# Optimization experiments

Measured on AMD Instinct MI355X. Metric: run time of the kernel, lower is better.

Reference implementation:

```python
import jax, jax.numpy as jnp
import numpy as np


def pw_dist_sq(X, Y):
    xx = jnp.sum(X * X, axis=1)[:, None]   # [N,1]
    yy = jnp.sum(Y * Y, axis=1)[None, :]   # [1,N]
    xy = X @ Y.T                            # [N,N]
    return jnp.maximum(xx + yy - 2.0 * xy, 0.0)


def setup_inputs() -> dict:
    key = jax.random.key(0)
    k1, k2 = jax.random.split(key)
    N, D = 1024, 128
    X = jax.random.normal(k1, (N, D), dtype=jnp.float32)
    Y = jax.random.normal(k2, (N, D), dtype=jnp.float32)
    return {"X": X, "Y": Y, "h": 1}


def reference(X, Y, h):
    h = float(h)
    inv_h2 = 1.0 / (h * h)
    sq_dists = pw_dist_sq(X, Y)                       # [N,N]
    K = jnp.exp(-0.5 * inv_h2 * sq_dists)             # [N,N]
    # d_K[i,j,:] = -(X[i]-Y[j])/h^2 * K[i,j]; returned reduced over j
    diff = X[:, None, :] - Y[None, :, :]              # [N,N,D]
    d_K_sum = jnp.sum(-diff * inv_h2 * K[:, :, None], axis=1)  # [N,D]
    return K, d_K_sum
```

## Files before the change

kernel.cpp:

```cpp
#include <hip/hip_runtime.h>

#define NN 1024
#define DD 128

typedef float f32x4 __attribute__((ext_vector_type(4)));
typedef _Float16 f16x8 __attribute__((ext_vector_type(8)));

__device__ __forceinline__ f16x8 cvt8(f32x4 a, f32x4 b) {
  f16x8 r;
  r[0] = (_Float16)a.x; r[1] = (_Float16)a.y; r[2] = (_Float16)a.z; r[3] = (_Float16)a.w;
  r[4] = (_Float16)b.x; r[5] = (_Float16)b.y; r[6] = (_Float16)b.z; r[7] = (_Float16)b.w;
  return r;
}

__global__ __launch_bounds__(256) void gk_fused(const float* __restrict__ X,
                                                const float* __restrict__ Y,
                                                const int* __restrict__ hp,
                                                float* __restrict__ out) {
  __shared__ __align__(16) float    Kt[16][132];
  __shared__ __align__(16) _Float16 Ks[16][136];
  __shared__ float yys[128];
  __shared__ unsigned msc[16];
  __shared__ float Sred[16];

  const int tid  = threadIdx.x;
  const int js   = blockIdx.x;
  const int ib   = blockIdx.y;
  const int lane = tid & 63;
  const int w    = tid >> 6;
  const int g    = lane >> 4;
  const int li   = lane & 15;

  const float fh = (float)hp[0];
  const float inv_h2 = 1.0f / (fh * fh);

  if (tid < 16) { msc[tid] = 0u; Sred[tid] = 0.0f; }

  const float* Xr = X + (size_t)(ib * 16 + li) * DD;
  f32x4 xa[4][2];
  float xx = 0.f;
  #pragma unroll
  for (int kt = 0; kt < 4; ++kt) {
    int d0 = kt * 32 + g * 8;
    xa[kt][0] = *(const f32x4*)(Xr + d0);
    xa[kt][1] = *(const f32x4*)(Xr + d0 + 4);
    #pragma unroll
    for (int c = 0; c < 4; ++c)
      xx += xa[kt][0][c] * xa[kt][0][c] + xa[kt][1][c] * xa[kt][1][c];
  }
  xx += __shfl_xor(xx, 16); xx += __shfl_xor(xx, 32);

  const float* Yr0 = Y + (size_t)(js * 128 + w * 32 + li) * DD;
  const float* Yr1 = Yr0 + 16 * DD;
  f32x4 acc0 = {0.f, 0.f, 0.f, 0.f}, acc1 = {0.f, 0.f, 0.f, 0.f};
  float yy0 = 0.f, yy1 = 0.f;
  #pragma unroll
  for (int kt = 0; kt < 4; ++kt) {
    int d0 = kt * 32 + g * 8;
    f32x4 a0 = *(const f32x4*)(Yr0 + d0), b0 = *(const f32x4*)(Yr0 + d0 + 4);
    f32x4 a1 = *(const f32x4*)(Yr1 + d0), b1 = *(const f32x4*)(Yr1 + d0 + 4);
    #pragma unroll
    for (int c = 0; c < 4; ++c) {
      yy0 += a0[c] * a0[c] + b0[c] * b0[c];
      yy1 += a1[c] * a1[c] + b1[c] * b1[c];
    }
    f16x8 bf = cvt8(xa[kt][0], xa[kt][1]);
    acc0 = __builtin_amdgcn_mfma_f32_16x16x32_f16(cvt8(a0, b0), bf, acc0, 0, 0, 0);
    acc1 = __builtin_amdgcn_mfma_f32_16x16x32_f16(cvt8(a1, b1), bf, acc1, 0, 0, 0);
  }
  yy0 += __shfl_xor(yy0, 16); yy0 += __shfl_xor(yy0, 32);
  yy1 += __shfl_xor(yy1, 16); yy1 += __shfl_xor(yy1, 32);
  if (lane < 16) { yys[w * 32 + lane] = yy0; yys[w * 32 + 16 + lane] = yy1; }
  __syncthreads();

  float K[8];
  float m = 0.f, sp = 0.f;
  #pragma unroll
  for (int t = 0; t < 2; ++t) {
    f32x4 a = t ? acc1 : acc0;
    #pragma unroll
    for (int r = 0; r < 4; ++r) {
      int jl = w * 32 + t * 16 + 4 * g + r;
      float e = fminf((a[r] - 0.5f * (xx + yys[jl])) * inv_h2, 0.0f);
      float kv = exp2f(e * 1.44269504088896341f);
      K[t * 4 + r] = kv; m = fmaxf(m, kv); sp += kv;
      Kt[li][jl] = kv;
    }
  }
  m = fmaxf(m, __shfl_xor(m, 16)); m = fmaxf(m, __shfl_xor(m, 32));
  sp += __shfl_xor(sp, 16);        sp += __shfl_xor(sp, 32);
  if (lane < 16) {
    atomicMax(&msc[li], __float_as_uint(m));
    atomicAdd(&Sred[li], sp);
  }
  __syncthreads();

  {
    int i = tid >> 4, seg = tid & 15;
    f32x4 v0 = *(const f32x4*)&Kt[i][seg * 8];
    f32x4 v1 = *(const f32x4*)&Kt[i][seg * 8 + 4];
    float* kb = out + (size_t)(ib * 16 + i) * NN + js * 128 + seg * 8;
    *(f32x4*)kb = v0; *(f32x4*)(kb + 4) = v1;
  }
  {
    unsigned ue = (msc[li] >> 23) & 0xffu;
    unsigned se = 266u - ue; if (se > 254u) se = 254u;
    float scale = __uint_as_float(se << 23);
    #pragma unroll
    for (int t = 0; t < 2; ++t)
      #pragma unroll
      for (int r = 0; r < 4; ++r)
        Ks[li][w * 32 + t * 16 + 4 * g + r] = (_Float16)(K[t * 4 + r] * scale);
  }
  __syncthreads();

  f32x4 c0 = {0.f, 0.f, 0.f, 0.f}, c1 = {0.f, 0.f, 0.f, 0.f};
  const int dA = w * 32 + li;
  const int dB = dA + 16;
  #pragma unroll
  for (int kt = 0; kt < 4; ++kt) {
    f16x8 af = *(const f16x8*)&Ks[li][kt * 32 + g * 8];
    const float* Yb = Y + (size_t)(js * 128 + kt * 32 + g * 8) * DD;
    f16x8 b0, b1;
    #pragma unroll
    for (int e = 0; e < 8; ++e) {
      b0[e] = (_Float16)Yb[e * DD + dA];
      b1[e] = (_Float16)Yb[e * DD + dB];
    }
    c0 = __builtin_amdgcn_mfma_f32_16x16x32_f16(af, b0, c0, 0, 0, 0);
    c1 = __builtin_amdgcn_mfma_f32_16x16x32_f16(af, b1, c1, 0, 0, 0);
  }

  float* dkp = out + (size_t)NN * NN;
  #pragma unroll
  for (int r = 0; r < 4; ++r) {
    int il = 4 * g + r;
    unsigned ue2 = (msc[il] >> 23) & 0xffu;
    unsigned se2 = 266u - ue2; if (se2 > 254u) se2 = 254u;
    float invs = __uint_as_float((254u - se2) << 23);
    float sred = Sred[il];
    int gi = ib * 16 + il;
    float x0 = X[(size_t)gi * DD + dA];
    float x1 = X[(size_t)gi * DD + dB];
    atomicAdd(dkp + (size_t)gi * DD + dA, (c0[r] * invs - sred * x0) * inv_h2);
    atomicAdd(dkp + (size_t)gi * DD + dB, (c1[r] * invs - sred * x1) * inv_h2);
  }
}

extern "C" void kernel_launch(void* const* d_in, const int* in_sizes, int n_in,
                              void* d_out, int out_size, void* d_ws, size_t ws_size,
                              hipStream_t stream) {
  const float* X  = (const float*)d_in[0];
  const float* Y  = (const float*)d_in[1];
  const int*   hp = (const int*)d_in[2];
  float* out = (float*)d_out;

  hipMemsetAsync((void*)(out + (size_t)NN * NN), 0, (size_t)NN * DD * sizeof(float), stream);
  hipLaunchKernelGGL(gk_fused, dim3(8, 64), dim3(256), 0, stream, X, Y, hp, out);
}
```

Before: 20.71 us.

## Replace memset and atomic dK accumulation with workspace partials and reduce kernel

The memset and the global atomicAdd accumulation of d_K_sum are removed. Each block now writes per-column-tile partial products and row sums to a workspace, and a second kernel reduces the 8 partials and applies the X correction. The change also prefetches the Y operand for the second GEMM early, stores K straight from registers instead of staging it through shared memory, and vectorizes the fp16 shared-memory stores. It trades atomic contention and the memset for an extra launch plus about 4MB of workspace traffic.

Measured after the change: 17.36 us. 16.2% less time.

```diff
diff --git a/kernel.cpp b/kernel.cpp
--- a/kernel.cpp
+++ b/kernel.cpp
@@ -4,6 +4,7 @@
 #define DD 128
 
 typedef float f32x4 __attribute__((ext_vector_type(4)));
+typedef _Float16 f16x4 __attribute__((ext_vector_type(4)));
 typedef _Float16 f16x8 __attribute__((ext_vector_type(8)));
 
 __device__ __forceinline__ f16x8 cvt8(f32x4 a, f32x4 b) {
@@ -13,11 +14,13 @@
   return r;
 }
 
-__global__ __launch_bounds__(256) void gk_fused(const float* __restrict__ X,
-                                                const float* __restrict__ Y,
-                                                const int* __restrict__ hp,
-                                                float* __restrict__ out) {
-  __shared__ __align__(16) float    Kt[16][132];
+#define WS_PART 8192
+
+__global__ __launch_bounds__(256, 2) void gk_main(const float* __restrict__ X,
+                                                  const float* __restrict__ Y,
+                                                  const int* __restrict__ hp,
+                                                  float* __restrict__ out,
+                                                  float* __restrict__ ws) {
   __shared__ __align__(16) _Float16 Ks[16][136];
   __shared__ float yys[128];
   __shared__ unsigned msc[16];
@@ -38,16 +41,31 @@
 
   const float* Xr = X + (size_t)(ib * 16 + li) * DD;
   f32x4 xa[4][2];
-  float xx = 0.f;
   #pragma unroll
   for (int kt = 0; kt < 4; ++kt) {
     int d0 = kt * 32 + g * 8;
     xa[kt][0] = *(const f32x4*)(Xr + d0);
     xa[kt][1] = *(const f32x4*)(Xr + d0 + 4);
+  }
+  const int dA = w * 32 + li;
+  const int dB = dA + 16;
+  float bpre0[4][8], bpre1[4][8];
+  #pragma unroll
+  for (int kt = 0; kt < 4; ++kt) {
+    const float* Yb = Y + (size_t)(js * 128 + kt * 32 + g * 8) * DD;
+    #pragma unroll
+    for (int e = 0; e < 8; ++e) {
+      bpre0[kt][e] = Yb[e * DD + dA];
+      bpre1[kt][e] = Yb[e * DD + dB];
+    }
+  }
+
+  float xx = 0.f;
+  #pragma unroll
+  for (int kt = 0; kt < 4; ++kt)
     #pragma unroll
     for (int c = 0; c < 4; ++c)
       xx += xa[kt][0][c] * xa[kt][0][c] + xa[kt][1][c] * xa[kt][1][c];
-  }
   xx += __shfl_xor(xx, 16); xx += __shfl_xor(xx, 32);
 
   const float* Yr0 = Y + (size_t)(js * 128 + w * 32 + li) * DD;
@@ -84,8 +102,14 @@
       float e = fminf((a[r] - 0.5f * (xx + yys[jl])) * inv_h2, 0.0f);
       float kv = exp2f(e * 1.44269504088896341f);
       K[t * 4 + r] = kv; m = fmaxf(m, kv); sp += kv;
-      Kt[li][jl] = kv;
-    }
+    }
+  }
+  {
+    float* kb = out + (size_t)(ib * 16 + li) * NN + js * 128 + w * 32 + 4 * g;
+    f32x4 k0 = { K[0], K[1], K[2], K[3] };
+    f32x4 k1 = { K[4], K[5], K[6], K[7] };
+    *(f32x4*)kb = k0;
+    *(f32x4*)(kb + 16) = k1;
   }
   m = fmaxf(m, __shfl_xor(m, 16)); m = fmaxf(m, __shfl_xor(m, 32));
   sp += __shfl_xor(sp, 16);        sp += __shfl_xor(sp, 32);
@@ -96,55 +120,71 @@
   __syncthreads();
 
   {
-    int i = tid >> 4, seg = tid & 15;
-    f32x4 v0 = *(const f32x4*)&Kt[i][seg * 8];
-    f32x4 v1 = *(const f32x4*)&Kt[i][seg * 8 + 4];
-    float* kb = out + (size_t)(ib * 16 + i) * NN + js * 128 + seg * 8;
-    *(f32x4*)kb = v0; *(f32x4*)(kb + 4) = v1;
-  }
-  {
     unsigned ue = (msc[li] >> 23) & 0xffu;
     unsigned se = 266u - ue; if (se > 254u) se = 254u;
     float scale = __uint_as_float(se << 23);
     #pragma unroll
-    for (int t = 0; t < 2; ++t)
+    for (int t = 0; t < 2; ++t) {
+      f16x4 q;
       #pragma unroll
-      for (int r = 0; r < 4; ++r)
-        Ks[li][w * 32 + t * 16 + 4 * g + r] = (_Float16)(K[t * 4 + r] * scale);
+      for (int r = 0; r < 4; ++r) q[r] = (_Float16)(K[t * 4 + r] * scale);
+      *(f16x4*)&Ks[li][w * 32 + t * 16 + 4 * g] = q;
+    }
   }
   __syncthreads();
 
   f32x4 c0 = {0.f, 0.f, 0.f, 0.f}, c1 = {0.f, 0.f, 0.f, 0.f};
-  const int dA = w * 32 + li;
-  const int dB = dA + 16;
   #pragma unroll
   for (int kt = 0; kt < 4; ++kt) {
     f16x8 af = *(const f16x8*)&Ks[li][kt * 32 + g * 8];
-    const float* Yb = Y + (size_t)(js * 128 + kt * 32 + g * 8) * DD;
     f16x8 b0, b1;
     #pragma unroll
     for (int e = 0; e < 8; ++e) {
-      b0[e] = (_Float16)Yb[e * DD + dA];
-      b1[e] = (_Float16)Yb[e * DD + dB];
+      b0[e] = (_Float16)bpre0[kt][e];
+      b1[e] = (_Float16)bpre1[kt][e];
     }
     c0 = __builtin_amdgcn_mfma_f32_16x16x32_f16(af, b0, c0, 0, 0, 0);
     c1 = __builtin_amdgcn_mfma_f32_16x16x32_f16(af, b1, c1, 0, 0, 0);
   }
 
-  float* dkp = out + (size_t)NN * NN;
+  float* pb = ws + WS_PART + (size_t)js * (NN * DD) + (size_t)(ib * 16) * DD;
   #pragma unroll
   for (int r = 0; r < 4; ++r) {
     int il = 4 * g + r;
     unsigned ue2 = (msc[il] >> 23) & 0xffu;
     unsigned se2 = 266u - ue2; if (se2 > 254u) se2 = 254u;
     float invs = __uint_as_float((254u - se2) << 23);
-    float sred = Sred[il];
-    int gi = ib * 16 + il;
-    float x0 = X[(size_t)gi * DD + dA];
-    float x1 = X[(size_t)gi * DD + dB];
-    atomicAdd(dkp + (size_t)gi * DD + dA, (c0[r] * invs - sred * x0) * inv_h2);
-    atomicAdd(dkp + (size_t)gi * DD + dB, (c1[r] * invs - sred * x1) * inv_h2);
-  }
+    pb[il * DD + dA] = c0[r] * invs;
+    pb[il * DD + dB] = c1[r] * invs;
+  }
+  if (tid < 16) ws[js * NN + ib * 16 + tid] = Sred[tid];
+}
+
+__global__ __launch_bounds__(256) void dk_reduce(const float* __restrict__ X,
+                                                 const int* __restrict__ hp,
+                                                 const float* __restrict__ ws,
+                                                 float* __restrict__ out) {
+  const int unit = blockIdx.x * 256 + threadIdx.x;
+  const int i  = unit >> 5;
+  const int d0 = (unit & 31) * 4;
+  const float fh = (float)hp[0];
+  const float inv_h2 = 1.0f / (fh * fh);
+
+  f32x4 acc = {0.f, 0.f, 0.f, 0.f};
+  float s = 0.f;
+  #pragma unroll
+  for (int js = 0; js < 8; ++js) {
+    f32x4 p = *(const f32x4*)(ws + WS_PART + (size_t)js * (NN * DD) + (size_t)i * DD + d0);
+    acc.x += p.x; acc.y += p.y; acc.z += p.z; acc.w += p.w;
+    s += ws[js * NN + i];
+  }
+  f32x4 xv = *(const f32x4*)(X + (size_t)i * DD + d0);
+  f32x4 r;
+  r.x = (acc.x - s * xv.x) * inv_h2;
+  r.y = (acc.y - s * xv.y) * inv_h2;
+  r.z = (acc.z - s * xv.z) * inv_h2;
+  r.w = (acc.w - s * xv.w) * inv_h2;
+  *(f32x4*)(out + (size_t)NN * NN + (size_t)i * DD + d0) = r;
 }
 
 extern "C" void kernel_launch(void* const* d_in, const int* in_sizes, int n_in,
@@ -154,7 +194,8 @@
   const float* Y  = (const float*)d_in[1];
   const int*   hp = (const int*)d_in[2];
   float* out = (float*)d_out;
-
-  hipMemsetAsync((void*)(out + (size_t)NN * NN), 0, (size_t)NN * DD * sizeof(float), stream);
-  hipLaunchKernelGGL(gk_fused, dim3(8, 64), dim3(256), 0, stream, X, Y, hp, out);
-}
+  float* ws  = (float*)d_ws;
+
+  hipLaunchKernelGGL(gk_main, dim3(8, 64), dim3(256), 0, stream, X, Y, hp, out, ws);
+  hipLaunchKernelGGL(dk_reduce, dim3(128), dim3(256), 0, stream, X, hp, ws, out);
+}
```
